# Performance work log

Hardware: AMD Instinct MI355X
Metric: run time of the kernel (lower is better)

The kernel has to match this reference:

```python
import jax, jax.numpy as jnp
import numpy as np

B, V, K, D, E, NE = 32, 512, 16, 128, 32, 8192


def setup_inputs() -> dict:
    key = jax.random.key(0)
    ks = jax.random.split(key, 12)
    s = 0.05
    return {
        "vertex_features": jax.random.normal(ks[0], (B, V, D), jnp.float32),
        "atom_adj": jax.random.randint(ks[1], (B * V * K,), 0, B * V),
        "bond_adj": jax.random.randint(ks[2], (B * V * K,), 0, B * NE),
        "h0": jax.random.normal(ks[3], (B, V, D), jnp.float32),
        "lamda": jnp.full((1,), 0.5, jnp.float32),
        "alpha": jnp.full((1,), 0.1, jnp.float32),
        "l": 1,
        "edge_initial": jax.random.normal(ks[4], (B, NE, E), jnp.float32),
        "vertex_mask": jnp.ones((B, V), jnp.float32),
        "nbs_mask": jax.random.uniform(ks[5], (B, V, K), jnp.float32),
        # label_U1: (D+E) -> D ; label_U2: 2D -> D ; feature_updating: D -> D (variant=False)
        "W1": jax.random.normal(ks[6], (D, D + E), jnp.float32) * s,
        "b1": jax.random.normal(ks[7], (D,), jnp.float32) * s,
        "W2": jax.random.normal(ks[8], (D, 2 * D), jnp.float32) * s,
        "b2": jax.random.normal(ks[9], (D,), jnp.float32) * s,
        "W3": jax.random.normal(ks[10], (D, D), jnp.float32) * s,
        "b3": jax.random.normal(ks[11], (D,), jnp.float32) * s,
    }


def reference(vertex_features, atom_adj, bond_adj, h0, lamda, alpha, l,
              edge_initial, vertex_mask, nbs_mask, W1, b1, W2, b2, W3, b3):
    b, v = vertex_mask.shape
    k = nbs_mask.shape[2]
    d = vertex_features.shape[-1]
    e = edge_initial.shape[-1]
    # gather neighbor vertex and edge features (flat index, torch.index_select semantics)
    vn = vertex_features.reshape(-1, d)[atom_adj].reshape(b, v, k, d)
    en = edge_initial.reshape(-1, e)[bond_adj].reshape(b, v, k, e)
    l_neighbor = jnp.concatenate([vn, en], axis=-1)            # [b,v,k,d+e]
    nl = jax.nn.gelu(l_neighbor @ W1.T + b1, approximate=False)  # exact GELU like torch F.gelu
    nl = jnp.sum(nl * nbs_mask[..., None], axis=-2)            # masked sum over neighbors -> [b,v,d]
    hi = jnp.concatenate([nl, vertex_features], axis=-1) @ W2.T + b2
    theta = jnp.log(lamda / l + 1.0)                           # broadcast scalar (shape [1])
    support = (1.0 - alpha) * hi + alpha * h0                  # variant=False: r == support
    out = theta * (support @ W3.T + b3) + (1.0 - theta) * support
    out = out + vertex_features                                # residual=True
    return out
```

## Files before the change

kernel.cpp:

```cpp
#include <hip/hip_runtime.h>
#include <hip/hip_bf16.h>
#include <math.h>

#define NLSTR 136
#define ASTR  168

typedef __bf16 bf16x8 __attribute__((ext_vector_type(8)));
typedef float f32x4 __attribute__((ext_vector_type(4)));
typedef float f32x16 __attribute__((ext_vector_type(16)));
typedef unsigned short ushort8v __attribute__((ext_vector_type(8)));

union FragU { ushort8v u; bf16x8 b; };

static __device__ inline unsigned short f2bf(float f){
  unsigned u = __float_as_uint(f);
  u += 0x7fffu + ((u >> 16) & 1u);
  return (unsigned short)(u >> 16);
}
static __device__ inline float bf2f(unsigned short u){
  return __uint_as_float(((unsigned)u) << 16);
}
static __device__ inline unsigned pk2(float a, float b){
  union { __hip_bfloat162 h; unsigned u; } r;
  r.h = __float22bfloat162_rn(float2{a, b});
  return r.u;
}
static __device__ inline ushort8v pkcvt8(float4 a, float4 b){
  union { unsigned u[4]; ushort8v v; } r;
  r.u[0] = pk2(a.x, a.y); r.u[1] = pk2(a.z, a.w);
  r.u[2] = pk2(b.x, b.y); r.u[3] = pk2(b.z, b.w);
  return r.v;
}

static __device__ inline float gelu_f(float x){
  float u = x * x;
  float p = fmaf(u, 0.07135481283f, 1.5957691216f);
  float t = x * p;
  float e = __builtin_amdgcn_exp2f(t * -1.44269504f);
  return x * __builtin_amdgcn_rcpf(1.0f + e);
}

#define WG_BARRIER() asm volatile("s_waitcnt lgkmcnt(0)\n\ts_barrier" ::: "memory")

__global__ __launch_bounds__(256) void prep_kernel(
    const float* __restrict__ vf, const float* __restrict__ W1,
    const float* __restrict__ W2, const float* __restrict__ W3,
    unsigned short* __restrict__ vfbf, unsigned short* __restrict__ w1f,
    unsigned short* __restrict__ w2f, unsigned short* __restrict__ w3f)
{
  int t = blockIdx.x * 256 + threadIdx.x;
  if (t < 262144){
    const float4* src = (const float4*)vf;
    float4 x = src[t * 2], y = src[t * 2 + 1];
    *(ushort8v*)(vfbf + t * 8) = pkcvt8(x, y);
    return;
  }
  int t2 = t - 262144;
  const float* s;
  unsigned short* d;
  if (t2 < 2560){
    int fragid = t2 >> 6, lane = t2 & 63;
    int nc2 = fragid / 10, kc = fragid % 10, n = lane & 31, h = lane >> 5;
    s = W1 + (nc2 * 32 + n) * 160 + kc * 16 + h * 8;
    d = w1f + t2 * 8;
  } else if (t2 < 6656){
    int t3 = t2 - 2560;
    int fragid = t3 >> 6, lane = t3 & 63;
    int kc = fragid >> 3, nc = fragid & 7, col = lane & 15, quad = lane >> 4;
    s = W2 + (nc * 16 + col) * 256 + kc * 32 + quad * 8;
    d = w2f + t3 * 8;
  } else if (t2 < 8704){
    int t3 = t2 - 6656;
    int fragid = t3 >> 6, lane = t3 & 63;
    int kc = fragid >> 3, nc = fragid & 7, col = lane & 15, quad = lane >> 4;
    s = W3 + (nc * 16 + col) * 128 + kc * 32 + quad * 8;
    d = w3f + t3 * 8;
  } else return;
#pragma unroll
  for (int j = 0; j < 8; j++) d[j] = f2bf(s[j]);
}

__global__ __launch_bounds__(256) void fused_kernel(
    const unsigned short* __restrict__ vfbf,
    const float* __restrict__ vf,
    const int* __restrict__ aadj, const int* __restrict__ badj,
    const float* __restrict__ edge, const float* __restrict__ nbs,
    const float* __restrict__ h0,
    const unsigned short* __restrict__ w1f, const unsigned short* __restrict__ w2f,
    const unsigned short* __restrict__ w3f,
    const float* __restrict__ b1, const float* __restrict__ b2, const float* __restrict__ b3,
    const float* __restrict__ lamda, const float* __restrict__ alpha,
    const int* __restrict__ lval,
    float* __restrict__ out)
{
  __shared__ __align__(16) unsigned short abuf[2][32 * ASTR];
  __shared__ __align__(16) unsigned short nl_lds[16 * NLSTR];
  __shared__ __align__(16) unsigned short sup_lds[16 * NLSTR];
  __shared__ __align__(16) float nbs_lds[256];
  const int wid  = threadIdx.x >> 6;
  const int lane = threadIdx.x & 63;
  const int n32  = lane & 31;
  const int h    = lane >> 5;
  const int col  = lane & 15;
  const int quad = lane >> 4;
  const int v0   = blockIdx.x * 16;

  const int srow = threadIdx.x >> 3;
  const int ssub = threadIdx.x & 7;

  nbs_lds[threadIdx.x] = nbs[v0 * 16 + threadIdx.x];

  int a_all[8], e_all[8];
  {
    const int base = (v0 + (srow >> 4)) * 16 + (srow & 15);
#pragma unroll
    for (int p = 0; p < 8; p++){
      a_all[p] = aadj[base + 32 * p];
      e_all[p] = badj[base + 32 * p];
    }
  }

  FragU bw[10];
#pragma unroll
  for (int kc = 0; kc < 10; kc++)
    bw[kc].u = *(const ushort8v*)(w1f + ((wid * 10 + kc) * 64 + lane) * 8);

  const float bb1 = b1[wid * 32 + n32];

  ushort8v sv0, sv1; float4 se;
  {
    const ushort8v* vs = (const ushort8v*)(vfbf + (size_t)a_all[0] * 128 + ssub * 16);
    sv0 = vs[0]; sv1 = vs[1];
    se = *(const float4*)(edge + (size_t)e_all[0] * 32 + ssub * 4);
  }
  {
    unsigned short* dst = abuf[0] + srow * ASTR + ssub * 16;
    *(ushort8v*)dst = sv0; *(ushort8v*)(dst + 8) = sv1;
    unsigned* ed = (unsigned*)(abuf[0] + srow * ASTR + 128 + ssub * 4);
    ed[0] = pk2(se.x, se.y); ed[1] = pk2(se.z, se.w);
  }
  {
    const ushort8v* vs = (const ushort8v*)(vfbf + (size_t)a_all[1] * 128 + ssub * 16);
    sv0 = vs[0]; sv1 = vs[1];
    se = *(const float4*)(edge + (size_t)e_all[1] * 32 + ssub * 4);
  }

#pragma unroll
  for (int p = 0; p < 8; ++p){
    WG_BARRIER();

    if (p < 7){
      unsigned short* dst = abuf[(p + 1) & 1] + srow * ASTR + ssub * 16;
      *(ushort8v*)dst = sv0; *(ushort8v*)(dst + 8) = sv1;
      unsigned* ed = (unsigned*)(abuf[(p + 1) & 1] + srow * ASTR + 128 + ssub * 4);
      ed[0] = pk2(se.x, se.y); ed[1] = pk2(se.z, se.w);
    }
    if (p < 6){
      const ushort8v* vs = (const ushort8v*)(vfbf + (size_t)a_all[p + 2] * 128 + ssub * 16);
      sv0 = vs[0]; sv1 = vs[1];
      se = *(const float4*)(edge + (size_t)e_all[p + 2] * 32 + ssub * 4);
    }

    const float4* nbsl = (const float4*)nbs_lds;
    const float4 mAlo = nbsl[8 * p + h],     mAhi = nbsl[8 * p + 2 + h];
    const float4 mBlo = nbsl[8 * p + 4 + h], mBhi = nbsl[8 * p + 6 + h];

    const unsigned short* ab = abuf[p & 1] + n32 * ASTR + h * 8;
    f32x16 accA = {}, accB = {};
#pragma unroll
    for (int kc = 0; kc < 10; kc += 2){
      FragU fa0, fa1;
      fa0.u = *(const ushort8v*)(ab + kc * 16);
      fa1.u = *(const ushort8v*)(ab + (kc + 1) * 16);
      accA = __builtin_amdgcn_mfma_f32_32x32x16_bf16(fa0.b, bw[kc].b,     accA, 0, 0, 0);
      accB = __builtin_amdgcn_mfma_f32_32x32x16_bf16(fa1.b, bw[kc + 1].b, accB, 0, 0, 0);
    }
    f32x16 acc = accA + accB;

    {
      float sA = gelu_f(acc[0] + bb1) * mAlo.x + gelu_f(acc[1] + bb1) * mAlo.y
               + gelu_f(acc[2] + bb1) * mAlo.z + gelu_f(acc[3] + bb1) * mAlo.w
               + gelu_f(acc[4] + bb1) * mAhi.x + gelu_f(acc[5] + bb1) * mAhi.y
               + gelu_f(acc[6] + bb1) * mAhi.z + gelu_f(acc[7] + bb1) * mAhi.w;
      float sB = gelu_f(acc[8] + bb1) * mBlo.x + gelu_f(acc[9] + bb1) * mBlo.y
               + gelu_f(acc[10] + bb1) * mBlo.z + gelu_f(acc[11] + bb1) * mBlo.w
               + gelu_f(acc[12] + bb1) * mBhi.x + gelu_f(acc[13] + bb1) * mBhi.y
               + gelu_f(acc[14] + bb1) * mBhi.z + gelu_f(acc[15] + bb1) * mBhi.w;
      sA += __shfl_xor(sA, 32, 64);
      sB += __shfl_xor(sB, 32, 64);
      if (h == 0) nl_lds[(2 * p)     * NLSTR + wid * 32 + n32] = f2bf(sA);
      else        nl_lds[(2 * p + 1) * NLSTR + wid * 32 + n32] = f2bf(sB);
    }
  }
  __syncthreads();

  const int nc0 = 2 * wid;
  const float th = logf(lamda[0] / (float)lval[0] + 1.0f);
  const float al = alpha[0];

  float h0v[2][4];
#pragma unroll
  for (int pq = 0; pq < 2; pq++){
    const int d = (nc0 + pq) * 16 + col;
#pragma unroll
    for (int r = 0; r < 4; r++)
      h0v[pq][r] = h0[(v0 + quad * 4 + r) * 128 + d];
  }

  f32x4 acc2[2] = {};
#pragma unroll
  for (int kc = 0; kc < 8; kc++){
    FragU a;
    if (kc < 4) a.u = *(const ushort8v*)(nl_lds + col * NLSTR + kc * 32 + quad * 8);
    else        a.u = *(const ushort8v*)(vfbf + (size_t)(v0 + col) * 128 + (kc - 4) * 32 + quad * 8);
#pragma unroll
    for (int pq = 0; pq < 2; pq++){
      FragU bf_;
      bf_.u = *(const ushort8v*)(w2f + ((kc * 8 + nc0 + pq) * 64 + lane) * 8);
      acc2[pq] = __builtin_amdgcn_mfma_f32_16x16x32_bf16(a.b, bf_.b, acc2[pq], 0, 0, 0);
    }
  }

  float sup[2][4];
#pragma unroll
  for (int pq = 0; pq < 2; pq++){
    const int d = (nc0 + pq) * 16 + col;
    const float bb = b2[d];
#pragma unroll
    for (int r = 0; r < 4; r++){
      float hi = acc2[pq][r] + bb;
      float s = (1.f - al) * hi + al * h0v[pq][r];
      sup[pq][r] = s;
      sup_lds[(quad * 4 + r) * NLSTR + d] = f2bf(s);
    }
  }
  __syncthreads();

  float rv[2][4];
#pragma unroll
  for (int pq = 0; pq < 2; pq++){
    const int d = (nc0 + pq) * 16 + col;
#pragma unroll
    for (int r = 0; r < 4; r++)
      rv[pq][r] = vf[(size_t)(v0 + quad * 4 + r) * 128 + d];
  }

  f32x4 acc3[2] = {};
#pragma unroll
  for (int kc = 0; kc < 4; kc++){
    FragU a;
    a.u = *(const ushort8v*)(sup_lds + col * NLSTR + kc * 32 + quad * 8);
#pragma unroll
    for (int pq = 0; pq < 2; pq++){
      FragU bf_;
      bf_.u = *(const ushort8v*)(w3f + ((kc * 8 + nc0 + pq) * 64 + lane) * 8);
      acc3[pq] = __builtin_amdgcn_mfma_f32_16x16x32_bf16(a.b, bf_.b, acc3[pq], 0, 0, 0);
    }
  }

#pragma unroll
  for (int pq = 0; pq < 2; pq++){
    const int d = (nc0 + pq) * 16 + col;
    const float bb = b3[d];
#pragma unroll
    for (int r = 0; r < 4; r++){
      const int vtx = v0 + quad * 4 + r;
      out[vtx * 128 + d] = th * (acc3[pq][r] + bb) + (1.f - th) * sup[pq][r] + rv[pq][r];
    }
  }
}

extern "C" void kernel_launch(void* const* d_in, const int* in_sizes, int n_in,
                              void* d_out, int out_size, void* d_ws, size_t ws_size,
                              hipStream_t stream)
{
  const float* vfp  = (const float*)d_in[0];
  const int*   aadj = (const int*)d_in[1];
  const int*   badj = (const int*)d_in[2];
  const float* h0   = (const float*)d_in[3];
  const float* lam  = (const float*)d_in[4];
  const float* alp  = (const float*)d_in[5];
  const int*   lv   = (const int*)d_in[6];
  const float* edge = (const float*)d_in[7];
  const float* nbs  = (const float*)d_in[9];
  const float* W1   = (const float*)d_in[10];
  const float* b1   = (const float*)d_in[11];
  const float* W2   = (const float*)d_in[12];
  const float* b2   = (const float*)d_in[13];
  const float* W3   = (const float*)d_in[14];
  const float* b3   = (const float*)d_in[15];
  float* out = (float*)d_out;

  unsigned short* w1f  = (unsigned short*)d_ws;
  unsigned short* w2f  = w1f + 20480;
  unsigned short* w3f  = w2f + 32768;
  unsigned short* vfbf = w3f + 16384;

  prep_kernel<<<1058, 256, 0, stream>>>(vfp, W1, W2, W3, vfbf, w1f, w2f, w3f);
  fused_kernel<<<1024, 256, 0, stream>>>(vfbf, vfp, aadj, badj, edge, nbs, h0,
                                         w1f, w2f, w3f, b1, b2, b3, lam, alp, lv, out);
}
```

Baseline: 138.1 us.

## Batch neighbor gathers into two phases of four buffers with fewer barriers

Replaces the double-buffered 8-step gather/MFMA pipeline with two phases, each issuing four neighbor gathers at once into a four-slot LDS buffer. The second batch of global loads is issued before the first batch is computed. The goal is more memory-level parallelism and fewer workgroup barriers, and the occupancy hint is raised to 3 blocks per CU. In exchange it needs more LDS and more registers to hold the in-flight gathers, which may reduce occupancy or cause spills.

```diff
diff --git a/kernel.cpp b/kernel.cpp
--- a/kernel.cpp
+++ b/kernel.cpp
@@ -80,7 +80,7 @@
   for (int j = 0; j < 8; j++) d[j] = f2bf(s[j]);
 }
 
-__global__ __launch_bounds__(256) void fused_kernel(
+__global__ __launch_bounds__(256, 3) void fused_kernel(
     const unsigned short* __restrict__ vfbf,
     const float* __restrict__ vf,
     const int* __restrict__ aadj, const int* __restrict__ badj,
@@ -93,7 +93,7 @@
     const int* __restrict__ lval,
     float* __restrict__ out)
 {
-  __shared__ __align__(16) unsigned short abuf[2][32 * ASTR];
+  __shared__ __align__(16) unsigned short abuf[4][32 * ASTR];
   __shared__ __align__(16) unsigned short nl_lds[16 * NLSTR];
   __shared__ __align__(16) unsigned short sup_lds[16 * NLSTR];
   __shared__ __align__(16) float nbs_lds[256];
@@ -108,8 +108,6 @@
   const int srow = threadIdx.x >> 3;
   const int ssub = threadIdx.x & 7;
 
-  nbs_lds[threadIdx.x] = nbs[v0 * 16 + threadIdx.x];
-
   int a_all[8], e_all[8];
   {
     const int base = (v0 + (srow >> 4)) * 16 + (srow & 15);
@@ -120,6 +118,16 @@
     }
   }
 
+  ushort8v sv[4][2]; float4 se[4];
+#pragma unroll
+  for (int q = 0; q < 4; q++){
+    const ushort8v* vs = (const ushort8v*)(vfbf + (size_t)a_all[q] * 128 + ssub * 16);
+    sv[q][0] = vs[0]; sv[q][1] = vs[1];
+    se[q] = *(const float4*)(edge + (size_t)e_all[q] * 32 + ssub * 4);
+  }
+
+  nbs_lds[threadIdx.x] = nbs[v0 * 16 + threadIdx.x];
+
   FragU bw[10];
 #pragma unroll
   for (int kc = 0; kc < 10; kc++)
@@ -127,45 +135,29 @@
 
   const float bb1 = b1[wid * 32 + n32];
 
-  ushort8v sv0, sv1; float4 se;
-  {
-    const ushort8v* vs = (const ushort8v*)(vfbf + (size_t)a_all[0] * 128 + ssub * 16);
-    sv0 = vs[0]; sv1 = vs[1];
-    se = *(const float4*)(edge + (size_t)e_all[0] * 32 + ssub * 4);
-  }
-  {
-    unsigned short* dst = abuf[0] + srow * ASTR + ssub * 16;
-    *(ushort8v*)dst = sv0; *(ushort8v*)(dst + 8) = sv1;
-    unsigned* ed = (unsigned*)(abuf[0] + srow * ASTR + 128 + ssub * 4);
-    ed[0] = pk2(se.x, se.y); ed[1] = pk2(se.z, se.w);
-  }
-  {
-    const ushort8v* vs = (const ushort8v*)(vfbf + (size_t)a_all[1] * 128 + ssub * 16);
-    sv0 = vs[0]; sv1 = vs[1];
-    se = *(const float4*)(edge + (size_t)e_all[1] * 32 + ssub * 4);
-  }
-
-#pragma unroll
-  for (int p = 0; p < 8; ++p){
-    WG_BARRIER();
-
-    if (p < 7){
-      unsigned short* dst = abuf[(p + 1) & 1] + srow * ASTR + ssub * 16;
-      *(ushort8v*)dst = sv0; *(ushort8v*)(dst + 8) = sv1;
-      unsigned* ed = (unsigned*)(abuf[(p + 1) & 1] + srow * ASTR + 128 + ssub * 4);
-      ed[0] = pk2(se.x, se.y); ed[1] = pk2(se.z, se.w);
-    }
-    if (p < 6){
-      const ushort8v* vs = (const ushort8v*)(vfbf + (size_t)a_all[p + 2] * 128 + ssub * 16);
-      sv0 = vs[0]; sv1 = vs[1];
-      se = *(const float4*)(edge + (size_t)e_all[p + 2] * 32 + ssub * 4);
-    }
-
-    const float4* nbsl = (const float4*)nbs_lds;
+#pragma unroll
+  for (int q = 0; q < 4; q++){
+    unsigned short* dst = abuf[q] + srow * ASTR + ssub * 16;
+    *(ushort8v*)dst = sv[q][0]; *(ushort8v*)(dst + 8) = sv[q][1];
+    unsigned* ed = (unsigned*)(abuf[q] + srow * ASTR + 128 + ssub * 4);
+    ed[0] = pk2(se[q].x, se[q].y); ed[1] = pk2(se[q].z, se[q].w);
+  }
+  WG_BARRIER();
+
+#pragma unroll
+  for (int q = 0; q < 4; q++){
+    const ushort8v* vs = (const ushort8v*)(vfbf + (size_t)a_all[q + 4] * 128 + ssub * 16);
+    sv[q][0] = vs[0]; sv[q][1] = vs[1];
+    se[q] = *(const float4*)(edge + (size_t)e_all[q + 4] * 32 + ssub * 4);
+  }
+
+  const float4* nbsl = (const float4*)nbs_lds;
+
+#pragma unroll
+  for (int p = 0; p < 4; p++){
     const float4 mAlo = nbsl[8 * p + h],     mAhi = nbsl[8 * p + 2 + h];
     const float4 mBlo = nbsl[8 * p + 4 + h], mBhi = nbsl[8 * p + 6 + h];
-
-    const unsigned short* ab = abuf[p & 1] + n32 * ASTR + h * 8;
+    const unsigned short* ab = abuf[p] + n32 * ASTR + h * 8;
     f32x16 accA = {}, accB = {};
 #pragma unroll
     for (int kc = 0; kc < 10; kc += 2){
@@ -176,21 +168,58 @@
       accB = __builtin_amdgcn_mfma_f32_32x32x16_bf16(fa1.b, bw[kc + 1].b, accB, 0, 0, 0);
     }
     f32x16 acc = accA + accB;
-
-    {
-      float sA = gelu_f(acc[0] + bb1) * mAlo.x + gelu_f(acc[1] + bb1) * mAlo.y
-               + gelu_f(acc[2] + bb1) * mAlo.z + gelu_f(acc[3] + bb1) * mAlo.w
-               + gelu_f(acc[4] + bb1) * mAhi.x + gelu_f(acc[5] + bb1) * mAhi.y
-               + gelu_f(acc[6] + bb1) * mAhi.z + gelu_f(acc[7] + bb1) * mAhi.w;
-      float sB = gelu_f(acc[8] + bb1) * mBlo.x + gelu_f(acc[9] + bb1) * mBlo.y
-               + gelu_f(acc[10] + bb1) * mBlo.z + gelu_f(acc[11] + bb1) * mBlo.w
-               + gelu_f(acc[12] + bb1) * mBhi.x + gelu_f(acc[13] + bb1) * mBhi.y
-               + gelu_f(acc[14] + bb1) * mBhi.z + gelu_f(acc[15] + bb1) * mBhi.w;
-      sA += __shfl_xor(sA, 32, 64);
-      sB += __shfl_xor(sB, 32, 64);
-      if (h == 0) nl_lds[(2 * p)     * NLSTR + wid * 32 + n32] = f2bf(sA);
-      else        nl_lds[(2 * p + 1) * NLSTR + wid * 32 + n32] = f2bf(sB);
-    }
+    float sA = gelu_f(acc[0] + bb1) * mAlo.x + gelu_f(acc[1] + bb1) * mAlo.y
+             + gelu_f(acc[2] + bb1) * mAlo.z + gelu_f(acc[3] + bb1) * mAlo.w
+             + gelu_f(acc[4] + bb1) * mAhi.x + gelu_f(acc[5] + bb1) * mAhi.y
+             + gelu_f(acc[6] + bb1) * mAhi.z + gelu_f(acc[7] + bb1) * mAhi.w;
+    float sB = gelu_f(acc[8] + bb1) * mBlo.x + gelu_f(acc[9] + bb1) * mBlo.y
+             + gelu_f(acc[10] + bb1) * mBlo.z + gelu_f(acc[11] + bb1) * mBlo.w
+             + gelu_f(acc[12] + bb1) * mBhi.x + gelu_f(acc[13] + bb1) * mBhi.y
+             + gelu_f(acc[14] + bb1) * mBhi.z + gelu_f(acc[15] + bb1) * mBhi.w;
+    sA += __shfl_xor(sA, 32, 64);
+    sB += __shfl_xor(sB, 32, 64);
+    if (h == 0) nl_lds[(2 * p)     * NLSTR + wid * 32 + n32] = f2bf(sA);
+    else        nl_lds[(2 * p + 1) * NLSTR + wid * 32 + n32] = f2bf(sB);
+  }
+  WG_BARRIER();
+
+#pragma unroll
+  for (int q = 0; q < 4; q++){
+    unsigned short* dst = abuf[q] + srow * ASTR + ssub * 16;
+    *(ushort8v*)dst = sv[q][0]; *(ushort8v*)(dst + 8) = sv[q][1];
+    unsigned* ed = (unsigned*)(abuf[q] + srow * ASTR + 128 + ssub * 4);
+    ed[0] = pk2(se[q].x, se[q].y); ed[1] = pk2(se[q].z, se[q].w);
+  }
+  WG_BARRIER();
+
+#pragma unroll
+  for (int p = 0; p < 4; p++){
+    const int pp = p + 4;
+    const float4 mAlo = nbsl[8 * pp + h],     mAhi = nbsl[8 * pp + 2 + h];
+    const float4 mBlo = nbsl[8 * pp + 4 + h], mBhi = nbsl[8 * pp + 6 + h];
+    const unsigned short* ab = abuf[p] + n32 * ASTR + h * 8;
+    f32x16 accA = {}, accB = {};
+#pragma unroll
+    for (int kc = 0; kc < 10; kc += 2){
+      FragU fa0, fa1;
+      fa0.u = *(const ushort8v*)(ab + kc * 16);
+      fa1.u = *(const ushort8v*)(ab + (kc + 1) * 16);
+      accA = __builtin_amdgcn_mfma_f32_32x32x16_bf16(fa0.b, bw[kc].b,     accA, 0, 0, 0);
+      accB = __builtin_amdgcn_mfma_f32_32x32x16_bf16(fa1.b, bw[kc + 1].b, accB, 0, 0, 0);
+    }
+    f32x16 acc = accA + accB;
+    float sA = gelu_f(acc[0] + bb1) * mAlo.x + gelu_f(acc[1] + bb1) * mAlo.y
+             + gelu_f(acc[2] + bb1) * mAlo.z + gelu_f(acc[3] + bb1) * mAlo.w
+             + gelu_f(acc[4] + bb1) * mAhi.x + gelu_f(acc[5] + bb1) * mAhi.y
+             + gelu_f(acc[6] + bb1) * mAhi.z + gelu_f(acc[7] + bb1) * mAhi.w;
+    float sB = gelu_f(acc[8] + bb1) * mBlo.x + gelu_f(acc[9] + bb1) * mBlo.y
+             + gelu_f(acc[10] + bb1) * mBlo.z + gelu_f(acc[11] + bb1) * mBlo.w
+             + gelu_f(acc[12] + bb1) * mBhi.x + gelu_f(acc[13] + bb1) * mBhi.y
+             + gelu_f(acc[14] + bb1) * mBhi.z + gelu_f(acc[15] + bb1) * mBhi.w;
+    sA += __shfl_xor(sA, 32, 64);
+    sB += __shfl_xor(sB, 32, 64);
+    if (h == 0) nl_lds[(2 * pp)     * NLSTR + wid * 32 + n32] = f2bf(sA);
+    else        nl_lds[(2 * pp + 1) * NLSTR + wid * 32 + n32] = f2bf(sB);
   }
   __syncthreads();
 
```

After: 136.0 us (median of 2 runs). Within noise of the previous version (-1.5%).

## Deepen gather prefetch to three stages and simplify MFMA/GELU chain

Applied to the files above, without the earlier changes.

Neighbor vertex/edge gathers are now prefetched three stages ahead in a register ring buffer instead of two, and the initial gathers are issued before the weight-fragment loads so more global-memory latency is hidden. The GELU approximation folds the log2e scaling into the polynomial constants, saving a multiply per element. The dual accumulator MFMA chain is collapsed into a single accumulator, and launch bounds request 4 blocks per CU. The extra prefetch registers and occupancy hint may increase register pressure or cause spills, and a single accumulator serializes the MFMA dependency chain.

```diff
diff --git a/kernel.cpp b/kernel.cpp
--- a/kernel.cpp
+++ b/kernel.cpp
@@ -34,9 +34,8 @@
 
 static __device__ inline float gelu_f(float x){
   float u = x * x;
-  float p = fmaf(u, 0.07135481283f, 1.5957691216f);
-  float t = x * p;
-  float e = __builtin_amdgcn_exp2f(t * -1.44269504f);
+  float p = fmaf(u, -0.1029434273f, -2.3022084765f);
+  float e = __builtin_amdgcn_exp2f(x * p);
   return x * __builtin_amdgcn_rcpf(1.0f + e);
 }
 
@@ -80,7 +79,7 @@
   for (int j = 0; j < 8; j++) d[j] = f2bf(s[j]);
 }
 
-__global__ __launch_bounds__(256) void fused_kernel(
+__global__ __launch_bounds__(256, 4) void fused_kernel(
     const unsigned short* __restrict__ vfbf,
     const float* __restrict__ vf,
     const int* __restrict__ aadj, const int* __restrict__ badj,
@@ -120,6 +119,14 @@
     }
   }
 
+  ushort8v sv[3][2]; float4 se[3];
+#pragma unroll
+  for (int s = 0; s < 3; s++){
+    const ushort8v* vs = (const ushort8v*)(vfbf + (size_t)a_all[s] * 128 + ssub * 16);
+    sv[s][0] = vs[0]; sv[s][1] = vs[1];
+    se[s] = *(const float4*)(edge + (size_t)e_all[s] * 32 + ssub * 4);
+  }
+
   FragU bw[10];
 #pragma unroll
   for (int kc = 0; kc < 10; kc++)
@@ -127,55 +134,44 @@
 
   const float bb1 = b1[wid * 32 + n32];
 
-  ushort8v sv0, sv1; float4 se;
-  {
-    const ushort8v* vs = (const ushort8v*)(vfbf + (size_t)a_all[0] * 128 + ssub * 16);
-    sv0 = vs[0]; sv1 = vs[1];
-    se = *(const float4*)(edge + (size_t)e_all[0] * 32 + ssub * 4);
-  }
   {
     unsigned short* dst = abuf[0] + srow * ASTR + ssub * 16;
-    *(ushort8v*)dst = sv0; *(ushort8v*)(dst + 8) = sv1;
+    *(ushort8v*)dst = sv[0][0]; *(ushort8v*)(dst + 8) = sv[0][1];
     unsigned* ed = (unsigned*)(abuf[0] + srow * ASTR + 128 + ssub * 4);
-    ed[0] = pk2(se.x, se.y); ed[1] = pk2(se.z, se.w);
-  }
-  {
-    const ushort8v* vs = (const ushort8v*)(vfbf + (size_t)a_all[1] * 128 + ssub * 16);
-    sv0 = vs[0]; sv1 = vs[1];
-    se = *(const float4*)(edge + (size_t)e_all[1] * 32 + ssub * 4);
-  }
+    ed[0] = pk2(se[0].x, se[0].y); ed[1] = pk2(se[0].z, se[0].w);
+  }
+
+  const float4* nbsl = (const float4*)nbs_lds;
 
 #pragma unroll
   for (int p = 0; p < 8; ++p){
     WG_BARRIER();
 
     if (p < 7){
+      const int s = (p + 1) % 3;
       unsigned short* dst = abuf[(p + 1) & 1] + srow * ASTR + ssub * 16;
-      *(ushort8v*)dst = sv0; *(ushort8v*)(dst + 8) = sv1;
+      *(ushort8v*)dst = sv[s][0]; *(ushort8v*)(dst + 8) = sv[s][1];
       unsigned* ed = (unsigned*)(abuf[(p + 1) & 1] + srow * ASTR + 128 + ssub * 4);
-      ed[0] = pk2(se.x, se.y); ed[1] = pk2(se.z, se.w);
-    }
-    if (p < 6){
-      const ushort8v* vs = (const ushort8v*)(vfbf + (size_t)a_all[p + 2] * 128 + ssub * 16);
-      sv0 = vs[0]; sv1 = vs[1];
-      se = *(const float4*)(edge + (size_t)e_all[p + 2] * 32 + ssub * 4);
-    }
-
-    const float4* nbsl = (const float4*)nbs_lds;
+      ed[0] = pk2(se[s].x, se[s].y); ed[1] = pk2(se[s].z, se[s].w);
+    }
+    if (p < 5){
+      const int s = (p + 3) % 3;
+      const ushort8v* vs = (const ushort8v*)(vfbf + (size_t)a_all[p + 3] * 128 + ssub * 16);
+      sv[s][0] = vs[0]; sv[s][1] = vs[1];
+      se[s] = *(const float4*)(edge + (size_t)e_all[p + 3] * 32 + ssub * 4);
+    }
+
     const float4 mAlo = nbsl[8 * p + h],     mAhi = nbsl[8 * p + 2 + h];
     const float4 mBlo = nbsl[8 * p + 4 + h], mBhi = nbsl[8 * p + 6 + h];
 
     const unsigned short* ab = abuf[p & 1] + n32 * ASTR + h * 8;
-    f32x16 accA = {}, accB = {};
-#pragma unroll
-    for (int kc = 0; kc < 10; kc += 2){
-      FragU fa0, fa1;
-      fa0.u = *(const ushort8v*)(ab + kc * 16);
-      fa1.u = *(const ushort8v*)(ab + (kc + 1) * 16);
-      accA = __builtin_amdgcn_mfma_f32_32x32x16_bf16(fa0.b, bw[kc].b,     accA, 0, 0, 0);
-      accB = __builtin_amdgcn_mfma_f32_32x32x16_bf16(fa1.b, bw[kc + 1].b, accB, 0, 0, 0);
-    }
-    f32x16 acc = accA + accB;
+    f32x16 acc = {};
+#pragma unroll
+    for (int kc = 0; kc < 10; kc++){
+      FragU fa;
+      fa.u = *(const ushort8v*)(ab + kc * 16);
+      acc = __builtin_amdgcn_mfma_f32_32x32x16_bf16(fa.b, bw[kc].b, acc, 0, 0, 0);
+    }
 
     {
       float sA = gelu_f(acc[0] + bb1) * mAlo.x + gelu_f(acc[1] + bb1) * mAlo.y
```

Measured after the change: 137.0 us. About the same (-0.7%).

## Halve vertices per block, fold bias into accumulator, and simplify GELU

Applied to the files above, without the earlier changes.

Each block now handles 8 vertices instead of 16, which doubles the grid to 2048 blocks. The second and third GEMMs duplicate rows (col&7), and only half of the quads write results. The first GEMM now uses a single accumulator chain seeded with the bias, runs under raised wave priority, and the GELU constants are folded so one multiply is removed. A launch-bounds occupancy hint of 6 is added. The intent is more parallelism and less ALU work in exchange for wasted MFMA work in the tail GEMMs, more redundant weight-fragment loads per vertex, and a longer dependent MFMA chain.

```diff
diff --git a/kernel.cpp b/kernel.cpp
--- a/kernel.cpp
+++ b/kernel.cpp
@@ -34,9 +34,8 @@
 
 static __device__ inline float gelu_f(float x){
   float u = x * x;
-  float p = fmaf(u, 0.07135481283f, 1.5957691216f);
-  float t = x * p;
-  float e = __builtin_amdgcn_exp2f(t * -1.44269504f);
+  float p = fmaf(u, -0.1029434273f, -2.3022084765f);
+  float e = __builtin_amdgcn_exp2f(x * p);
   return x * __builtin_amdgcn_rcpf(1.0f + e);
 }
 
@@ -80,7 +79,7 @@
   for (int j = 0; j < 8; j++) d[j] = f2bf(s[j]);
 }
 
-__global__ __launch_bounds__(256) void fused_kernel(
+__global__ __launch_bounds__(256, 6) void fused_kernel(
     const unsigned short* __restrict__ vfbf,
     const float* __restrict__ vf,
     const int* __restrict__ aadj, const int* __restrict__ badj,
@@ -94,27 +93,27 @@
     float* __restrict__ out)
 {
   __shared__ __align__(16) unsigned short abuf[2][32 * ASTR];
-  __shared__ __align__(16) unsigned short nl_lds[16 * NLSTR];
-  __shared__ __align__(16) unsigned short sup_lds[16 * NLSTR];
-  __shared__ __align__(16) float nbs_lds[256];
+  __shared__ __align__(16) unsigned short nl_lds[8 * NLSTR];
+  __shared__ __align__(16) unsigned short sup_lds[8 * NLSTR];
+  __shared__ __align__(16) float nbs_lds[128];
   const int wid  = threadIdx.x >> 6;
   const int lane = threadIdx.x & 63;
   const int n32  = lane & 31;
   const int h    = lane >> 5;
   const int col  = lane & 15;
   const int quad = lane >> 4;
-  const int v0   = blockIdx.x * 16;
+  const int v0   = blockIdx.x * 8;
 
   const int srow = threadIdx.x >> 3;
   const int ssub = threadIdx.x & 7;
 
-  nbs_lds[threadIdx.x] = nbs[v0 * 16 + threadIdx.x];
-
-  int a_all[8], e_all[8];
+  if (threadIdx.x < 128) nbs_lds[threadIdx.x] = nbs[v0 * 16 + threadIdx.x];
+
+  int a_all[4], e_all[4];
   {
     const int base = (v0 + (srow >> 4)) * 16 + (srow & 15);
 #pragma unroll
-    for (int p = 0; p < 8; p++){
+    for (int p = 0; p < 4; p++){
       a_all[p] = aadj[base + 32 * p];
       e_all[p] = badj[base + 32 * p];
     }
@@ -145,47 +144,49 @@
     se = *(const float4*)(edge + (size_t)e_all[1] * 32 + ssub * 4);
   }
 
-#pragma unroll
-  for (int p = 0; p < 8; ++p){
+  const float4* nbsl = (const float4*)nbs_lds;
+
+#pragma unroll
+  for (int p = 0; p < 4; ++p){
     WG_BARRIER();
 
-    if (p < 7){
+    if (p < 3){
       unsigned short* dst = abuf[(p + 1) & 1] + srow * ASTR + ssub * 16;
       *(ushort8v*)dst = sv0; *(ushort8v*)(dst + 8) = sv1;
       unsigned* ed = (unsigned*)(abuf[(p + 1) & 1] + srow * ASTR + 128 + ssub * 4);
       ed[0] = pk2(se.x, se.y); ed[1] = pk2(se.z, se.w);
     }
-    if (p < 6){
+    if (p < 2){
       const ushort8v* vs = (const ushort8v*)(vfbf + (size_t)a_all[p + 2] * 128 + ssub * 16);
       sv0 = vs[0]; sv1 = vs[1];
       se = *(const float4*)(edge + (size_t)e_all[p + 2] * 32 + ssub * 4);
     }
 
-    const float4* nbsl = (const float4*)nbs_lds;
     const float4 mAlo = nbsl[8 * p + h],     mAhi = nbsl[8 * p + 2 + h];
     const float4 mBlo = nbsl[8 * p + 4 + h], mBhi = nbsl[8 * p + 6 + h];
 
     const unsigned short* ab = abuf[p & 1] + n32 * ASTR + h * 8;
-    f32x16 accA = {}, accB = {};
-#pragma unroll
-    for (int kc = 0; kc < 10; kc += 2){
-      FragU fa0, fa1;
-      fa0.u = *(const ushort8v*)(ab + kc * 16);
-      fa1.u = *(const ushort8v*)(ab + (kc + 1) * 16);
-      accA = __builtin_amdgcn_mfma_f32_32x32x16_bf16(fa0.b, bw[kc].b,     accA, 0, 0, 0);
-      accB = __builtin_amdgcn_mfma_f32_32x32x16_bf16(fa1.b, bw[kc + 1].b, accB, 0, 0, 0);
-    }
-    f32x16 acc = accA + accB;
+    f32x16 acc;
+#pragma unroll
+    for (int j = 0; j < 16; j++) acc[j] = bb1;
+    __builtin_amdgcn_s_setprio(1);
+#pragma unroll
+    for (int kc = 0; kc < 10; kc++){
+      FragU fa;
+      fa.u = *(const ushort8v*)(ab + kc * 16);
+      acc = __builtin_amdgcn_mfma_f32_32x32x16_bf16(fa.b, bw[kc].b, acc, 0, 0, 0);
+    }
+    __builtin_amdgcn_s_setprio(0);
 
     {
-      float sA = gelu_f(acc[0] + bb1) * mAlo.x + gelu_f(acc[1] + bb1) * mAlo.y
-               + gelu_f(acc[2] + bb1) * mAlo.z + gelu_f(acc[3] + bb1) * mAlo.w
-               + gelu_f(acc[4] + bb1) * mAhi.x + gelu_f(acc[5] + bb1) * mAhi.y
-               + gelu_f(acc[6] + bb1) * mAhi.z + gelu_f(acc[7] + bb1) * mAhi.w;
-      float sB = gelu_f(acc[8] + bb1) * mBlo.x + gelu_f(acc[9] + bb1) * mBlo.y
-               + gelu_f(acc[10] + bb1) * mBlo.z + gelu_f(acc[11] + bb1) * mBlo.w
-               + gelu_f(acc[12] + bb1) * mBhi.x + gelu_f(acc[13] + bb1) * mBhi.y
-               + gelu_f(acc[14] + bb1) * mBhi.z + gelu_f(acc[15] + bb1) * mBhi.w;
+      float sA = fmaf(gelu_f(acc[0]), mAlo.x, gelu_f(acc[1]) * mAlo.y)
+               + fmaf(gelu_f(acc[2]), mAlo.z, gelu_f(acc[3]) * mAlo.w)
+               + fmaf(gelu_f(acc[4]), mAhi.x, gelu_f(acc[5]) * mAhi.y)
+               + fmaf(gelu_f(acc[6]), mAhi.z, gelu_f(acc[7]) * mAhi.w);
+      float sB = fmaf(gelu_f(acc[8]), mBlo.x, gelu_f(acc[9]) * mBlo.y)
+               + fmaf(gelu_f(acc[10]), mBlo.z, gelu_f(acc[11]) * mBlo.w)
+               + fmaf(gelu_f(acc[12]), mBhi.x, gelu_f(acc[13]) * mBhi.y)
+               + fmaf(gelu_f(acc[14]), mBhi.z, gelu_f(acc[15]) * mBhi.w);
       sA += __shfl_xor(sA, 32, 64);
       sB += __shfl_xor(sB, 32, 64);
       if (h == 0) nl_lds[(2 * p)     * NLSTR + wid * 32 + n32] = f2bf(sA);
@@ -197,6 +198,7 @@
   const int nc0 = 2 * wid;
   const float th = logf(lamda[0] / (float)lval[0] + 1.0f);
   const float al = alpha[0];
+  const int vrow = quad * 4;
 
   float h0v[2][4];
 #pragma unroll
@@ -204,15 +206,15 @@
     const int d = (nc0 + pq) * 16 + col;
 #pragma unroll
     for (int r = 0; r < 4; r++)
-      h0v[pq][r] = h0[(v0 + quad * 4 + r) * 128 + d];
+      h0v[pq][r] = h0[(v0 + ((vrow + r) & 7)) * 128 + d];
   }
 
   f32x4 acc2[2] = {};
 #pragma unroll
   for (int kc = 0; kc < 8; kc++){
     FragU a;
-    if (kc < 4) a.u = *(const ushort8v*)(nl_lds + col * NLSTR + kc * 32 + quad * 8);
-    else        a.u = *(const ushort8v*)(vfbf + (size_t)(v0 + col) * 128 + (kc - 4) * 32 + quad * 8);
+    if (kc < 4) a.u = *(const ushort8v*)(nl_lds + (col & 7) * NLSTR + kc * 32 + quad * 8);
+    else        a.u = *(const ushort8v*)(vfbf + (size_t)(v0 + (col & 7)) * 128 + (kc - 4) * 32 + quad * 8);
 #pragma unroll
     for (int pq = 0; pq < 2; pq++){
       FragU bf_;
@@ -231,7 +233,7 @@
       float hi = acc2[pq][r] + bb;
       float s = (1.f - al) * hi + al * h0v[pq][r];
       sup[pq][r] = s;
-      sup_lds[(quad * 4 + r) * NLSTR + d] = f2bf(s);
+      if (quad < 2) sup_lds[(vrow + r) * NLSTR + d] = f2bf(s);
     }
   }
   __syncthreads();
@@ -242,14 +244,14 @@
     const int d = (nc0 + pq) * 16 + col;
 #pragma unroll
     for (int r = 0; r < 4; r++)
-      rv[pq][r] = vf[(size_t)(v0 + quad * 4 + r) * 128 + d];
+      rv[pq][r] = vf[(size_t)(v0 + ((vrow + r) & 7)) * 128 + d];
   }
 
   f32x4 acc3[2] = {};
 #pragma unroll
   for (int kc = 0; kc < 4; kc++){
     FragU a;
-    a.u = *(const ushort8v*)(sup_lds + col * NLSTR + kc * 32 + quad * 8);
+    a.u = *(const ushort8v*)(sup_lds + (col & 7) * NLSTR + kc * 32 + quad * 8);
 #pragma unroll
     for (int pq = 0; pq < 2; pq++){
       FragU bf_;
@@ -258,14 +260,16 @@
     }
   }
 
-#pragma unroll
-  for (int pq = 0; pq < 2; pq++){
-    const int d = (nc0 + pq) * 16 + col;
-    const float bb = b3[d];
-#pragma unroll
-    for (int r = 0; r < 4; r++){
-      const int vtx = v0 + quad * 4 + r;
-      out[vtx * 128 + d] = th * (acc3[pq][r] + bb) + (1.f - th) * sup[pq][r] + rv[pq][r];
+  if (quad < 2){
+#pragma unroll
+    for (int pq = 0; pq < 2; pq++){
+      const int d = (nc0 + pq) * 16 + col;
+      const float bb = b3[d];
+#pragma unroll
+      for (int r = 0; r < 4; r++){
+        const int vtx = v0 + vrow + r;
+        out[vtx * 128 + d] = th * (acc3[pq][r] + bb) + (1.f - th) * sup[pq][r] + rv[pq][r];
+      }
     }
   }
 }
@@ -297,6 +301,6 @@
   unsigned short* vfbf = w3f + 16384;
 
   prep_kernel<<<1058, 256, 0, stream>>>(vfp, W1, W2, W3, vfbf, w1f, w2f, w3f);
-  fused_kernel<<<1024, 256, 0, stream>>>(vfbf, vfp, aadj, badj, edge, nbs, h0,
+  fused_kernel<<<2048, 256, 0, stream>>>(vfbf, vfp, aadj, badj, edge, nbs, h0,
                                          w1f, w2f, w3f, b1, b2, b3, lam, alp, lv, out);
 }
```

After: 227.6 us. 1.65x slower.
